# Kernel tuning notes

Measured on AMD Instinct MI355X. Metric: run time of the kernel, lower is better.

Reference implementation:

```python
import jax, jax.numpy as jnp
import numpy as np

D_FEATURE = 512
D_K = 512
B, LQ, N = 64, 128, 2048
NEG_BIAS = 1e10


def setup_inputs() -> dict:
    key = jax.random.key(0)
    k1, k2, k3, k4, k5, k6 = jax.random.split(key, 6)
    # xavier_uniform bound for Linear(d_feature -> d_k), weight shape [d_k, d_feature]
    bound = float(np.sqrt(6.0 / (D_FEATURE + D_K)))
    metal_feature = jax.random.normal(k1, (B, LQ, D_FEATURE), dtype=jnp.float32)
    x = jax.random.normal(k2, (B, N, D_FEATURE), dtype=jnp.float32)
    mask = jax.random.randint(k3, (B, N), 0, 2, dtype=jnp.int32)
    W_q = jax.random.uniform(k4, (D_K, D_FEATURE), jnp.float32, -bound, bound)
    W_k = jax.random.uniform(k5, (D_K, D_FEATURE), jnp.float32, -bound, bound)
    W_v = jax.random.uniform(k6, (D_K, D_FEATURE), jnp.float32, -bound, bound)
    return {"metal_feature": metal_feature, "x": x, "mask": mask,
            "W_q": W_q, "W_k": W_k, "W_v": W_v}


def reference(metal_feature, x, mask, W_q, W_k, W_v):
    # Q: [B, Lq, d_k], K/V: [B, N, d_k]  (torch Linear: y = x @ W.T, no bias)
    Q = jnp.einsum('blf,kf->blk', metal_feature, W_q)
    K = jnp.einsum('bnf,kf->bnk', x, W_k)
    V = jnp.einsum('bnf,kf->bnk', x, W_v)
    scale = 1.0 / jnp.sqrt(jnp.float32(D_K))
    # scores: [B, Lq, N] with additive mask bias (mask broadcast over queries)
    scores = jnp.einsum('blk,bnk->bln', Q, K) * scale
    scores = scores - (1.0 - mask[:, None, :].astype(scores.dtype)) * NEG_BIAS
    attn = jax.nn.softmax(scores, axis=-1)
    out = jnp.einsum('bln,bnk->blk', attn, V)
    # relu; squeeze(1) is a no-op for Lq>1; dropout identity at eval
    return jax.nn.relu(out)
```

## Files before the change

### kernel.cpp

```cpp
#include <hip/hip_runtime.h>

typedef __attribute__((ext_vector_type(4))) float   f32x4;
typedef __attribute__((ext_vector_type(4))) float   float4v;
typedef __attribute__((ext_vector_type(8))) __bf16  bf16x8;
typedef unsigned short u16;
typedef __attribute__((ext_vector_type(8))) unsigned short u16x8;
typedef __attribute__((ext_vector_type(4))) unsigned short u16x4;

__device__ __forceinline__ u16 f2bf(float f) {
  unsigned u = __builtin_bit_cast(unsigned, f);
  u += 0x7fffu + ((u >> 16) & 1u);
  return (u16)(u >> 16);
}
__device__ __forceinline__ float bf2f(u16 h) {
  unsigned u = ((unsigned)h) << 16;
  return __builtin_bit_cast(float, u);
}

#define BM 128
#define BN 128
#define BK 32
#define LDT 40

template<int AF32, int EPI>
__global__ __launch_bounds__(256)
void gemm_k(const void* __restrict__ Ap, const u16* __restrict__ Bp,
            void* __restrict__ Cp, void* __restrict__ Cp2,
            const int* __restrict__ maskp,
            int K, long sA, long sB, long sC, long sM, int ldc, float scale)
{
  __shared__ u16 As[2][BM * LDT];
  __shared__ u16 Bs[2][BM * LDT];

  const int t  = threadIdx.x;
  const int z  = blockIdx.z;
  const int n0 = blockIdx.x * BN;
  const int m0 = blockIdx.y * BM;
  const int KT = K / BK;

  const u16* Bb = Bp + (long)z * sB;

  f32x4 acc[4][4];
#pragma unroll
  for (int i = 0; i < 4; i++)
#pragma unroll
    for (int j = 0; j < 4; j++) acc[i][j] = f32x4{0.f, 0.f, 0.f, 0.f};

  const int w = t >> 6, lane = t & 63;
  const int m0w = (w >> 1) * 64, n0w = (w & 1) * 64;
  const int lr = lane & 15, lc = lane >> 4;

  float4v fa[4];
  u16x8   ua[2];
  u16x8   ub[2];

  auto loadA = [&](int kt) {
    if constexpr (AF32) {
      const float* A = (const float*)Ap + (long)z * sA;
#pragma unroll
      for (int i = 0; i < 4; i++) {
        int idx = i * 256 + t, r = idx >> 3, c4 = idx & 7;
        fa[i] = *(const float4v*)(A + (long)(m0 + r) * K + kt * BK + c4 * 4);
      }
    } else {
      const u16* A = (const u16*)Ap + (long)z * sA;
#pragma unroll
      for (int i = 0; i < 2; i++) {
        int idx = i * 256 + t, r = idx >> 2, c8 = idx & 3;
        ua[i] = *(const u16x8*)(A + (long)(m0 + r) * K + kt * BK + c8 * 8);
      }
    }
  };
  auto loadB = [&](int kt) {
#pragma unroll
    for (int i = 0; i < 2; i++) {
      int idx = i * 256 + t, r = idx >> 2, c8 = idx & 3;
      ub[i] = *(const u16x8*)(Bb + (long)(n0 + r) * K + kt * BK + c8 * 8);
    }
  };
  auto writeAB = [&](int buf) {
    if constexpr (AF32) {
#pragma unroll
      for (int i = 0; i < 4; i++) {
        int idx = i * 256 + t, r = idx >> 3, c4 = idx & 7;
        u16x4 h;
#pragma unroll
        for (int jj = 0; jj < 4; jj++) h[jj] = f2bf(fa[i][jj]);
        *(u16x4*)&As[buf][r * LDT + c4 * 4] = h;
      }
    } else {
#pragma unroll
      for (int i = 0; i < 2; i++) {
        int idx = i * 256 + t, r = idx >> 2, c8 = idx & 3;
        *(u16x8*)&As[buf][r * LDT + c8 * 8] = ua[i];
      }
    }
#pragma unroll
    for (int i = 0; i < 2; i++) {
      int idx = i * 256 + t, r = idx >> 2, c8 = idx & 3;
      *(u16x8*)&Bs[buf][r * LDT + c8 * 8] = ub[i];
    }
  };
  auto compute = [&](int buf) {
    bf16x8 af[4], bfr[4];
#pragma unroll
    for (int f = 0; f < 4; f++) {
      af[f]  = __builtin_bit_cast(bf16x8, *(const u16x8*)&As[buf][(m0w + f * 16 + lr) * LDT + lc * 8]);
      bfr[f] = __builtin_bit_cast(bf16x8, *(const u16x8*)&Bs[buf][(n0w + f * 16 + lr) * LDT + lc * 8]);
    }
#pragma unroll
    for (int i = 0; i < 4; i++)
#pragma unroll
      for (int j = 0; j < 4; j++)
        acc[i][j] = __builtin_amdgcn_mfma_f32_16x16x32_bf16(af[i], bfr[j], acc[i][j], 0, 0, 0);
  };

  loadA(0); loadB(0);
  writeAB(0);
  __syncthreads();
  int cur = 0;
  for (int kt = 1; kt < KT; ++kt) {
    loadA(kt); loadB(kt);
    compute(cur);
    writeAB(cur ^ 1);
    __syncthreads();
    cur ^= 1;
  }
  compute(cur);

#pragma unroll
  for (int i = 0; i < 4; i++) {
#pragma unroll
    for (int j = 0; j < 4; j++) {
      const int mb = m0 + m0w + i * 16 + lc * 4;
      const int n  = n0 + n0w + j * 16 + lr;
      if constexpr (EPI == 0) {
        u16* C = (u16*)Cp + (long)z * sC;
#pragma unroll
        for (int ii = 0; ii < 4; ii++)
          C[(long)(mb + ii) * ldc + n] = f2bf(acc[i][j][ii]);
      } else if constexpr (EPI == 1) {
        if (n < 512) {
          u16* C = (u16*)Cp;
#pragma unroll
          for (int ii = 0; ii < 4; ii++)
            C[(long)(mb + ii) * 512 + n] = f2bf(acc[i][j][ii]);
        } else {
          u16* C2 = (u16*)Cp2;
          const int b = mb >> 11, kv = mb & 2047, d = n - 512;
          u16x4 h;
#pragma unroll
          for (int ii = 0; ii < 4; ii++) h[ii] = f2bf(acc[i][j][ii]);
          *(u16x4*)(C2 + ((long)(b * 512 + d)) * 2048 + kv) = h;
        }
      } else if constexpr (EPI == 2) {
        const int* mk = maskp + (long)z * sM;
        u16* C = (u16*)Cp + (long)z * sC;
        const float bias = mk[n] ? 0.f : -1e10f;
#pragma unroll
        for (int ii = 0; ii < 4; ii++)
          C[(long)(mb + ii) * ldc + n] = f2bf(acc[i][j][ii] * scale + bias);
      } else {
        float* C = (float*)Cp + (long)z * sC;
#pragma unroll
        for (int ii = 0; ii < 4; ii++)
          C[(long)(mb + ii) * ldc + n] = fmaxf(acc[i][j][ii], 0.f);
      }
    }
  }
}

__global__ __launch_bounds__(256)
void wconv_k(const float* __restrict__ Wq, const float* __restrict__ Wk,
             const float* __restrict__ Wv, u16* __restrict__ Wb)
{
  long i4 = (long)blockIdx.x * 256 + threadIdx.x;
  long e  = i4 * 4;
  const float* W = (e < 262144) ? Wq : (e < 524288 ? Wk : Wv);
  long off = e & 262143;
  float4v f = *(const float4v*)(W + off);
  u16x4 h;
#pragma unroll
  for (int j = 0; j < 4; j++) h[j] = f2bf(f[j]);
  *(u16x4*)(Wb + e) = h;
}

__global__ __launch_bounds__(256)
void softmax_k(u16* __restrict__ S)
{
  const long row = blockIdx.x;
  const int  t   = threadIdx.x;
  u16* R = S + row * 2048;
  u16x8 v = *(const u16x8*)(R + t * 8);
  float f[8];
#pragma unroll
  for (int j = 0; j < 8; j++) f[j] = bf2f(v[j]);
  float m = f[0];
#pragma unroll
  for (int j = 1; j < 8; j++) m = fmaxf(m, f[j]);
#pragma unroll
  for (int off = 32; off > 0; off >>= 1) m = fmaxf(m, __shfl_xor(m, off));
  __shared__ float red[4], red2[4];
  const int w = t >> 6;
  if ((t & 63) == 0) red[w] = m;
  __syncthreads();
  m = fmaxf(fmaxf(red[0], red[1]), fmaxf(red[2], red[3]));
  float e[8], s = 0.f;
#pragma unroll
  for (int j = 0; j < 8; j++) { e[j] = __expf(f[j] - m); s += e[j]; }
#pragma unroll
  for (int off = 32; off > 0; off >>= 1) s += __shfl_xor(s, off);
  if ((t & 63) == 0) red2[w] = s;
  __syncthreads();
  s = red2[0] + red2[1] + red2[2] + red2[3];
  const float inv = 1.f / s;
  u16x8 o;
#pragma unroll
  for (int j = 0; j < 8; j++) o[j] = f2bf(e[j] * inv);
  *(u16x8*)(R + t * 8) = o;
}

extern "C" void kernel_launch(void* const* d_in, const int* in_sizes, int n_in,
                              void* d_out, int out_size, void* d_ws, size_t ws_size,
                              hipStream_t stream)
{
  const float* mf   = (const float*)d_in[0];
  const float* x    = (const float*)d_in[1];
  const int*   mask = (const int*)d_in[2];
  const float* Wq   = (const float*)d_in[3];
  const float* Wk   = (const float*)d_in[4];
  const float* Wv   = (const float*)d_in[5];
  float* out = (float*)d_out;

  u16* ws = (u16*)d_ws;
  u16* Wb = ws;
  u16* Qb = Wb + 786432;
  u16* dyn = Qb + 4194304;

  const size_t fixed_b = (size_t)(786432 + 4194304) * 2;
  int CB = 64;
  while (CB > 1 && fixed_b + (size_t)CB * 4718592ull > ws_size) CB >>= 1;

  u16* Kc  = dyn;
  u16* Vtc = Kc + (size_t)CB * 2048 * 512;
  u16* Sc  = Vtc + (size_t)CB * 512 * 2048;

  const float scale = 0.044194173824159216f;

  wconv_k<<<768, 256, 0, stream>>>(Wq, Wk, Wv, Wb);

  gemm_k<1, 0><<<dim3(4, 64, 1), 256, 0, stream>>>(
      mf, Wb, Qb, nullptr, nullptr, 512, 0, 0, 0, 0, 512, 1.f);

  for (int bc = 0; bc < 64; bc += CB) {
    const float* xc = x + (long)bc * 2048 * 512;
    gemm_k<1, 1><<<dim3(8, CB * 16, 1), 256, 0, stream>>>(
        xc, Wb + 262144, Kc, Vtc, nullptr, 512, 0, 0, 0, 0, 512, 1.f);
    gemm_k<0, 2><<<dim3(16, 1, CB), 256, 0, stream>>>(
        Qb + (long)bc * 65536, Kc, Sc, nullptr, mask + (long)bc * 2048,
        512, 65536, 1048576, 262144, 2048, 2048, scale);
    softmax_k<<<CB * 128, 256, 0, stream>>>(Sc);
    gemm_k<0, 3><<<dim3(4, 1, CB), 256, 0, stream>>>(
        Sc, Vtc, out + (long)bc * 65536, nullptr, nullptr,
        2048, 262144, 1048576, 65536, 0, 512, 1.f);
  }
}
```

Measured before the change: 474.7 us.

## Stage GEMM tiles with direct global-to-LDS loads, XOR swizzle, and grid remap

Replaces register-staged global loads plus LDS writes with global_load_lds direct copies into XOR-swizzled shared memory tiles. The fp32 A path now keeps fp32 in LDS and converts to bf16 at fragment-read time. The Q projection input is pre-converted to bf16 by a new cvt kernel. The K/V projection GEMM also gets a workgroup-index remap. The aim is to cut VGPR staging and LDS bank conflicts and to improve cache locality. In exchange it doubles LDS use for the fp32 tile, adds a kernel launch, and needs more workspace.

```diff
diff --git a/kernel.cpp b/kernel.cpp
--- a/kernel.cpp
+++ b/kernel.cpp
@@ -1,7 +1,6 @@
 #include <hip/hip_runtime.h>
 
 typedef __attribute__((ext_vector_type(4))) float   f32x4;
-typedef __attribute__((ext_vector_type(4))) float   float4v;
 typedef __attribute__((ext_vector_type(8))) __bf16  bf16x8;
 typedef unsigned short u16;
 typedef __attribute__((ext_vector_type(8))) unsigned short u16x8;
@@ -17,112 +16,111 @@
   return __builtin_bit_cast(float, u);
 }
 
-#define BM 128
-#define BN 128
-#define BK 32
-#define LDT 40
-
-template<int AF32, int EPI>
+__device__ __forceinline__ void gld16(const void* g, void* l) {
+  __builtin_amdgcn_global_load_lds(
+      (const __attribute__((address_space(1))) void*)g,
+      (__attribute__((address_space(3))) void*)l, 16, 0, 0);
+}
+
+template<int AF32, int EPI, int SWZ>
 __global__ __launch_bounds__(256)
 void gemm_k(const void* __restrict__ Ap, const u16* __restrict__ Bp,
             void* __restrict__ Cp, void* __restrict__ Cp2,
             const int* __restrict__ maskp,
             int K, long sA, long sB, long sC, long sM, int ldc, float scale)
 {
-  __shared__ u16 As[2][BM * LDT];
-  __shared__ u16 Bs[2][BM * LDT];
-
-  const int t  = threadIdx.x;
-  const int z  = blockIdx.z;
-  const int n0 = blockIdx.x * BN;
-  const int m0 = blockIdx.y * BM;
-  const int KT = K / BK;
-
+  __shared__ float Asf[2][AF32 ? 4096 : 4];
+  __shared__ u16   Asb[2][AF32 ? 4 : 4096];
+  __shared__ u16   Bs [2][4096];
+
+  int bx = blockIdx.x, by = blockIdx.y;
+  if constexpr (SWZ) {
+    int nwg = gridDim.x * gridDim.y;
+    int h = bx + gridDim.x * by;
+    int q = nwg >> 3;
+    int s = (h & 7) * q + (h >> 3);
+    bx = s % gridDim.x; by = s / gridDim.x;
+  }
+  const int t = threadIdx.x, z = blockIdx.z;
+  const int n0 = bx * 128, m0 = by * 128;
+  const int KT = K / 32;
   const u16* Bb = Bp + (long)z * sB;
-
-  f32x4 acc[4][4];
-#pragma unroll
-  for (int i = 0; i < 4; i++)
-#pragma unroll
-    for (int j = 0; j < 4; j++) acc[i][j] = f32x4{0.f, 0.f, 0.f, 0.f};
 
   const int w = t >> 6, lane = t & 63;
   const int m0w = (w >> 1) * 64, n0w = (w & 1) * 64;
   const int lr = lane & 15, lc = lane >> 4;
 
-  float4v fa[4];
-  u16x8   ua[2];
-  u16x8   ub[2];
-
-  auto loadA = [&](int kt) {
+  f32x4 acc[4][4];
+#pragma unroll
+  for (int i = 0; i < 4; i++)
+#pragma unroll
+    for (int j = 0; j < 4; j++) acc[i][j] = f32x4{0.f, 0.f, 0.f, 0.f};
+
+  auto stage = [&](int buf, int kt) {
     if constexpr (AF32) {
       const float* A = (const float*)Ap + (long)z * sA;
 #pragma unroll
       for (int i = 0; i < 4; i++) {
-        int idx = i * 256 + t, r = idx >> 3, c4 = idx & 7;
-        fa[i] = *(const float4v*)(A + (long)(m0 + r) * K + kt * BK + c4 * 4);
+        int chunk = w * 4 + i;
+        int row = chunk * 8 + (lane >> 3);
+        int cc  = lane & 7;
+        const float* g = A + (long)(m0 + row) * K + kt * 32 + ((cc ^ (row & 7)) << 2);
+        gld16(g, (void*)&Asf[buf][chunk * 256]);
       }
     } else {
       const u16* A = (const u16*)Ap + (long)z * sA;
 #pragma unroll
       for (int i = 0; i < 2; i++) {
-        int idx = i * 256 + t, r = idx >> 2, c8 = idx & 3;
-        ua[i] = *(const u16x8*)(A + (long)(m0 + r) * K + kt * BK + c8 * 8);
-      }
+        int chunk = w * 2 + i;
+        int row = chunk * 16 + (lane >> 2);
+        int cc  = lane & 3;
+        const u16* g = A + (long)(m0 + row) * K + kt * 32 + ((cc ^ ((row >> 1) & 3)) << 3);
+        gld16(g, (void*)&Asb[buf][chunk * 512]);
+      }
+    }
+#pragma unroll
+    for (int i = 0; i < 2; i++) {
+      int chunk = w * 2 + i;
+      int row = chunk * 16 + (lane >> 2);
+      int cc  = lane & 3;
+      const u16* g = Bb + (long)(n0 + row) * K + kt * 32 + ((cc ^ ((row >> 1) & 3)) << 3);
+      gld16(g, (void*)&Bs[buf][chunk * 512]);
     }
   };
-  auto loadB = [&](int kt) {
-#pragma unroll
-    for (int i = 0; i < 2; i++) {
-      int idx = i * 256 + t, r = idx >> 2, c8 = idx & 3;
-      ub[i] = *(const u16x8*)(Bb + (long)(n0 + r) * K + kt * BK + c8 * 8);
-    }
+
+  auto compute = [&](int buf) {
+    bf16x8 af[4], bv[4];
+#pragma unroll
+    for (int f = 0; f < 4; f++) {
+      const int R = m0w + f * 16 + lr;
+      if constexpr (AF32) {
+        f32x4 lo = *(const f32x4*)&Asf[buf][R * 32 + (((lc * 2 + 0) ^ (R & 7)) << 2)];
+        f32x4 hi = *(const f32x4*)&Asf[buf][R * 32 + (((lc * 2 + 1) ^ (R & 7)) << 2)];
+        bf16x8 v;
+#pragma unroll
+        for (int j = 0; j < 4; j++) { v[j] = (__bf16)lo[j]; v[4 + j] = (__bf16)hi[j]; }
+        af[f] = v;
+      } else {
+        af[f] = __builtin_bit_cast(bf16x8,
+            *(const u16x8*)&Asb[buf][R * 32 + ((lc ^ ((R >> 1) & 3)) << 3)]);
+      }
+      const int R2 = n0w + f * 16 + lr;
+      bv[f] = __builtin_bit_cast(bf16x8,
+          *(const u16x8*)&Bs[buf][R2 * 32 + ((lc ^ ((R2 >> 1) & 3)) << 3)]);
+    }
+#pragma unroll
+    for (int i = 0; i < 4; i++)
+#pragma unroll
+      for (int j = 0; j < 4; j++)
+        acc[i][j] = __builtin_amdgcn_mfma_f32_16x16x32_bf16(af[i], bv[j], acc[i][j], 0, 0, 0);
   };
-  auto writeAB = [&](int buf) {
-    if constexpr (AF32) {
-#pragma unroll
-      for (int i = 0; i < 4; i++) {
-        int idx = i * 256 + t, r = idx >> 3, c4 = idx & 7;
-        u16x4 h;
-#pragma unroll
-        for (int jj = 0; jj < 4; jj++) h[jj] = f2bf(fa[i][jj]);
-        *(u16x4*)&As[buf][r * LDT + c4 * 4] = h;
-      }
-    } else {
-#pragma unroll
-      for (int i = 0; i < 2; i++) {
-        int idx = i * 256 + t, r = idx >> 2, c8 = idx & 3;
-        *(u16x8*)&As[buf][r * LDT + c8 * 8] = ua[i];
-      }
-    }
-#pragma unroll
-    for (int i = 0; i < 2; i++) {
-      int idx = i * 256 + t, r = idx >> 2, c8 = idx & 3;
-      *(u16x8*)&Bs[buf][r * LDT + c8 * 8] = ub[i];
-    }
-  };
-  auto compute = [&](int buf) {
-    bf16x8 af[4], bfr[4];
-#pragma unroll
-    for (int f = 0; f < 4; f++) {
-      af[f]  = __builtin_bit_cast(bf16x8, *(const u16x8*)&As[buf][(m0w + f * 16 + lr) * LDT + lc * 8]);
-      bfr[f] = __builtin_bit_cast(bf16x8, *(const u16x8*)&Bs[buf][(n0w + f * 16 + lr) * LDT + lc * 8]);
-    }
-#pragma unroll
-    for (int i = 0; i < 4; i++)
-#pragma unroll
-      for (int j = 0; j < 4; j++)
-        acc[i][j] = __builtin_amdgcn_mfma_f32_16x16x32_bf16(af[i], bfr[j], acc[i][j], 0, 0, 0);
-  };
-
-  loadA(0); loadB(0);
-  writeAB(0);
+
+  stage(0, 0);
   __syncthreads();
   int cur = 0;
   for (int kt = 1; kt < KT; ++kt) {
-    loadA(kt); loadB(kt);
+    stage(cur ^ 1, kt);
     compute(cur);
-    writeAB(cur ^ 1);
     __syncthreads();
     cur ^= 1;
   }
@@ -178,11 +176,23 @@
   long e  = i4 * 4;
   const float* W = (e < 262144) ? Wq : (e < 524288 ? Wk : Wv);
   long off = e & 262143;
-  float4v f = *(const float4v*)(W + off);
+  f32x4 f = *(const f32x4*)(W + off);
   u16x4 h;
 #pragma unroll
   for (int j = 0; j < 4; j++) h[j] = f2bf(f[j]);
   *(u16x4*)(Wb + e) = h;
+}
+
+__global__ __launch_bounds__(256)
+void cvt_k(const float* __restrict__ in, u16* __restrict__ out)
+{
+  long i = ((long)blockIdx.x * 256 + threadIdx.x) * 8;
+  f32x4 a = *(const f32x4*)(in + i);
+  f32x4 b = *(const f32x4*)(in + i + 4);
+  u16x8 h;
+#pragma unroll
+  for (int j = 0; j < 4; j++) { h[j] = f2bf(a[j]); h[4 + j] = f2bf(b[j]); }
+  *(u16x8*)(out + i) = h;
 }
 
 __global__ __launch_bounds__(256)
@@ -232,35 +242,37 @@
   const float* Wv   = (const float*)d_in[5];
   float* out = (float*)d_out;
 
-  u16* ws = (u16*)d_ws;
-  u16* Wb = ws;
-  u16* Qb = Wb + 786432;
+  u16* ws  = (u16*)d_ws;
+  u16* Wb  = ws;
+  u16* mfb = Wb + 786432;
+  u16* Qb  = mfb + 4194304;
   u16* dyn = Qb + 4194304;
 
-  const size_t fixed_b = (size_t)(786432 + 4194304) * 2;
+  const size_t fixedB = (size_t)(786432 + 4194304 + 4194304) * 2;
   int CB = 64;
-  while (CB > 1 && fixed_b + (size_t)CB * 4718592ull > ws_size) CB >>= 1;
+  while (CB > 1 && fixedB + (size_t)CB * 4718592ull > ws_size) CB >>= 1;
 
   u16* Kc  = dyn;
-  u16* Vtc = Kc + (size_t)CB * 2048 * 512;
-  u16* Sc  = Vtc + (size_t)CB * 512 * 2048;
+  u16* Vtc = Kc + (size_t)CB * 1048576;
+  u16* Sc  = Vtc + (size_t)CB * 1048576;
 
   const float scale = 0.044194173824159216f;
 
   wconv_k<<<768, 256, 0, stream>>>(Wq, Wk, Wv, Wb);
-
-  gemm_k<1, 0><<<dim3(4, 64, 1), 256, 0, stream>>>(
-      mf, Wb, Qb, nullptr, nullptr, 512, 0, 0, 0, 0, 512, 1.f);
+  cvt_k<<<2048, 256, 0, stream>>>(mf, mfb);
+
+  gemm_k<0, 0, 0><<<dim3(4, 64, 1), 256, 0, stream>>>(
+      mfb, Wb, Qb, nullptr, nullptr, 512, 0, 0, 0, 0, 512, 1.f);
 
   for (int bc = 0; bc < 64; bc += CB) {
     const float* xc = x + (long)bc * 2048 * 512;
-    gemm_k<1, 1><<<dim3(8, CB * 16, 1), 256, 0, stream>>>(
+    gemm_k<1, 1, 1><<<dim3(8, CB * 16, 1), 256, 0, stream>>>(
         xc, Wb + 262144, Kc, Vtc, nullptr, 512, 0, 0, 0, 0, 512, 1.f);
-    gemm_k<0, 2><<<dim3(16, 1, CB), 256, 0, stream>>>(
+    gemm_k<0, 2, 0><<<dim3(16, 1, CB), 256, 0, stream>>>(
         Qb + (long)bc * 65536, Kc, Sc, nullptr, mask + (long)bc * 2048,
         512, 65536, 1048576, 262144, 2048, 2048, scale);
     softmax_k<<<CB * 128, 256, 0, stream>>>(Sc);
-    gemm_k<0, 3><<<dim3(4, 1, CB), 256, 0, stream>>>(
+    gemm_k<0, 3, 0><<<dim3(4, 1, CB), 256, 0, stream>>>(
         Sc, Vtc, out + (long)bc * 65536, nullptr, nullptr,
         2048, 262144, 1048576, 65536, 0, 512, 1.f);
   }
```

Result: no change. 474.4 us (-0.1%).
